# Optimization experiments

Hardware: AMD Instinct MI355X
Metric: run time of the kernel (lower is better)

The kernel has to match this reference:

```python
import jax, jax.numpy as jnp
import numpy as np


def setup_inputs() -> dict:
    key = jax.random.key(0)
    k1, k2, k3, k4 = jax.random.split(key, 4)
    B, L, P = 1024, 128, 32
    ctrl_latent = jax.random.normal(k1, (B, L), dtype=jnp.float32)
    pert_embedding = jax.random.normal(k2, (B, P), dtype=jnp.float32)
    # learned params (torch init is zeros; use small randn so grads/outputs are non-trivial)
    weights = jax.random.normal(k3, (L * P * P, L), dtype=jnp.float32) * 0.02
    bias = jax.random.normal(k4, (L,), dtype=jnp.float32) * 0.02
    return {"ctrl_latent": ctrl_latent, "pert_embedding": pert_embedding,
            "weights": weights, "bias": bias}


def reference(ctrl_latent, pert_embedding, weights, bias):
    # ctrl_latent: (B, L); pert_embedding: (B, P); weights: (L*P*P, L); bias: (L,)
    B = ctrl_latent.shape[0]
    # outer product of pert embedding with itself: (B, P, P) -> (B, P*P)
    inter = jnp.einsum('bi,bj->bij', pert_embedding, pert_embedding).reshape(B, -1)
    # full interaction with control latent: (B, L, P*P) -> (B, L*P*P)
    x = (ctrl_latent[:, :, None] * inter[:, None, :]).reshape(B, -1)
    # dropout is identity at inference
    return x @ weights + bias
```

## Files before the change

kernel.cpp:

```cpp
#include <hip/hip_runtime.h>
#include <hip/hip_bf16.h>
#include <hip/hip_fp16.h>

#define B_   1024
#define L_   128
#define P_   32
#define PP_  1024
#define N_   128
#define KP_  576
#define KT_  73728

typedef float    f32x4 __attribute__((ext_vector_type(4)));
typedef _Float16 f16x8 __attribute__((ext_vector_type(8)));
typedef _Float16 f16x2 __attribute__((ext_vector_type(2)));
typedef __fp16   fp16x2_builtin __attribute__((ext_vector_type(2)));

__device__ __constant__ unsigned char IJTAB[36] = {
  0,1,2,3,4,5,6,7, 9,10,11,12,13,14,15, 18,19,20,21,22,23,
  27,28,29,30,31, 36,37,38,39, 45,46,47, 54,55, 63};

static __device__ __forceinline__ unsigned int pk16(float a, float b) {
  fp16x2_builtin h = __builtin_amdgcn_cvt_pkrtz(a, b);
  return *(unsigned int*)&h;
}

static __device__ __forceinline__ void gload16(void* lds, const void* g) {
  __builtin_amdgcn_global_load_lds(
      (const __attribute__((address_space(1))) unsigned int*)g,
      (__attribute__((address_space(3))) unsigned int*)lds, 16, 0, 0);
}

__global__ __launch_bounds__(256) void prep_kernel(
    const float* __restrict__ W, const float* __restrict__ pert,
    unsigned short* __restrict__ Wt, uint4* __restrict__ interf)
{
  const int bid = blockIdx.x, tid = threadIdx.x;
  __shared__ unsigned int t32[32 * 133];
  if (bid < 1152) {
    const int q = bid & 127, grp = bid >> 7;
    const int l = (q & 63) * 2 + (q >> 6);
    const size_t baseL = (size_t)l * PP_;
    for (int i = 0; i < 4; ++i) {
      int idx = tid + i * 256;
      int sp = idx >> 5, nq = (idx & 31) * 4;
      const int s = grp * 64 + 2 * sp;
      const int blk = s >> 4, a = (s >> 2) & 3, c = (s >> 1) & 1;
      const int ij = IJTAB[blk], I = ij >> 3, J = ij & 7;
      const int rowX = (4 * I + a) * 32 + 4 * J + 2 * c;
      float4 s0 = *(const float4*)(W + (baseL + rowX)     * N_ + nq);
      float4 s1 = *(const float4*)(W + (baseL + rowX + 1) * N_ + nq);
      if (I != J) {
        const int rowY0 = (4 * J + 2 * c) * 32 + 4 * I + a;
        const float4 y0 = *(const float4*)(W + (baseL + rowY0)      * N_ + nq);
        const float4 y1 = *(const float4*)(W + (baseL + rowY0 + 32) * N_ + nq);
        s0.x += y0.x; s0.y += y0.y; s0.z += y0.z; s0.w += y0.w;
        s1.x += y1.x; s1.y += y1.y; s1.z += y1.z; s1.w += y1.w;
      }
      uint4 w;
      w.x = pk16(s0.x, s1.x);
      w.y = pk16(s0.y, s1.y);
      w.z = pk16(s0.z, s1.z);
      w.w = pk16(s0.w, s1.w);
      *(uint4*)&t32[sp * 133 + nq] = w;
    }
    __syncthreads();
    for (int i = 0; i < 4; ++i) {
      int idx = tid + i * 256;
      int n = idx >> 3, cg = idx & 7;
      uint4 w;
      w.x = t32[(cg * 4 + 0) * 133 + n];
      w.y = t32[(cg * 4 + 1) * 133 + n];
      w.z = t32[(cg * 4 + 2) * 133 + n];
      w.w = t32[(cg * 4 + 3) * 133 + n];
      *(uint4*)(Wt + (size_t)n * KT_ + l * KP_ + grp * 64 + cg * 8) = w;
    }
  } else {
    const int mt = bid - 1152;
    __shared__ float pl[512];
    pl[tid]       = pert[(size_t)mt * 512 + tid];
    pl[tid + 256] = pert[(size_t)mt * 512 + tid + 256];
    __syncthreads();
    for (int r = 0; r < 5; ++r) {
      const int idx = tid + r * 256;
      if (idx < 1152) {
        const int k8 = idx >> 4, lm = idx & 15;
        const int blk = k8 >> 1, a0 = 2 * (k8 & 1);
        const int ij = IJTAB[blk], I = ij >> 3, J = ij & 7;
        const float* p = &pl[lm * 32];
        const float pi0 = p[4 * I + a0], pi1 = p[4 * I + a0 + 1];
        const float* pj = p + 4 * J;
        uint4 w;
        w.x = pk16(pi0 * pj[0], pi0 * pj[1]);
        w.y = pk16(pi0 * pj[2], pi0 * pj[3]);
        w.z = pk16(pi1 * pj[0], pi1 * pj[1]);
        w.w = pk16(pi1 * pj[2], pi1 * pj[3]);
        interf[(size_t)mt * 1152 + idx] = w;
      }
    }
  }
}

__global__ __launch_bounds__(256, 2) void gemm_kernel(
    const unsigned short* __restrict__ Wt,
    const uint4* __restrict__ interf,
    const float* __restrict__ ctrl,
    _Float16* __restrict__ partials)
{
  __shared__ unsigned short Bsm[2][128 * 64];

  const int tid    = threadIdx.x;
  const int kchunk = blockIdx.x & 63;
  const int mtile  = blockIdx.x >> 6;
  const int m0     = mtile * 128;
  const int l0     = kchunk * 2;
  const int lane = tid & 63, wid = tid >> 6;
  const int wm = (wid >> 1) * 64, wn = (wid & 1) * 64;
  const int lm = lane & 15, kq = lane >> 4;

  const int srow = lane >> 3, c8 = lane & 7;
  const int sc = (c8 ^ srow) * 8;

  const unsigned short* bg0[4]; const unsigned short* bg1[4];
  unsigned short* bl0[4];       unsigned short* bl1[4];
  for (int j = 0; j < 4; ++j) {
    const int rr = wid * 32 + j * 8;
    bg0[j] = Wt + (size_t)(rr + srow) * KT_ + (size_t)l0 * KP_ + sc;
    bg1[j] = bg0[j] + KP_;
    bl0[j] = &Bsm[0][rr * 64];
    bl1[j] = &Bsm[1][rr * 64];
  }

  const uint4* ap[4];
  for (int tm = 0; tm < 4; ++tm)
    ap[tm] = interf + (size_t)(mtile * 8 + (wid >> 1) * 4 + tm) * 1152 + lane;

  f32x4 acc[2][4][4];
  for (int li = 0; li < 2; ++li)
    for (int tm = 0; tm < 4; ++tm)
      for (int tn = 0; tn < 4; ++tn)
        acc[li][tm][tn] = (f32x4){0.f, 0.f, 0.f, 0.f};

  for (int it = 0; it < 9; ++it) {
    const int q0 = it * 64;
    __syncthreads();
    f16x8 af[2][4];
    for (int ks = 0; ks < 2; ++ks)
      for (int tm = 0; tm < 4; ++tm)
        af[ks][tm] = *(const f16x8*)(ap[tm] + it * 128 + ks * 64);
    for (int j = 0; j < 4; ++j) gload16(bl0[j], bg0[j] + q0);
    for (int j = 0; j < 4; ++j) gload16(bl1[j], bg1[j] + q0);
    __syncthreads();
    for (int ks = 0; ks < 2; ++ks) {
      const int ch = (((ks * 4 + kq) ^ (lm & 7)) * 8);
      for (int li = 0; li < 2; ++li) {
        f16x8 bfr[4];
        for (int t = 0; t < 4; ++t)
          bfr[t] = *(const f16x8*)&Bsm[li][(wn + t * 16 + lm) * 64 + ch];
        for (int tm = 0; tm < 4; ++tm)
          for (int t = 0; t < 4; ++t)
            acc[li][tm][t] = __builtin_amdgcn_mfma_f32_16x16x32_f16(
                af[ks][tm], bfr[t], acc[li][tm][t], 0, 0, 0);
      }
    }
  }

  _Float16* pb = partials + (size_t)blockIdx.x * (128 * 128);
  for (int tm = 0; tm < 4; ++tm)
    for (int reg = 0; reg < 4; ++reg) {
      const int row = wm + tm * 16 + kq * 4 + reg;
      const float c0v = ctrl[(size_t)(m0 + row) * L_ + l0];
      const float c1v = ctrl[(size_t)(m0 + row) * L_ + l0 + 1];
      for (int tn = 0; tn < 4; ++tn)
        pb[row * 128 + wn + tn * 16 + lm] = (_Float16)(
            c0v * acc[0][tm][tn][reg] + c1v * acc[1][tm][tn][reg]);
    }
}

__global__ __launch_bounds__(256) void reduce_kernel(
    const _Float16* __restrict__ partials, const float* __restrict__ bias,
    float* __restrict__ out)
{
  __shared__ float red[4][64][2];
  const int bid = blockIdx.x;
  const int mtile = bid >> 7, row = bid & 127;
  const int tid = threadIdx.x, lane = tid & 63, w = tid >> 6;
  const _Float16* base = partials + ((size_t)(mtile * 64)) * 16384
                         + row * 128 + lane * 2;
  float s0 = 0.f, s1 = 0.f;
  #pragma unroll 8
  for (int i = 0; i < 16; ++i) {
    const int sp = w + i * 4;
    f16x2 v = *(const f16x2*)(base + ((size_t)sp << 14));
    s0 += (float)v[0];
    s1 += (float)v[1];
  }
  red[w][lane][0] = s0;
  red[w][lane][1] = s1;
  __syncthreads();
  if (w == 0) {
    float r0 = red[0][lane][0] + red[1][lane][0] + red[2][lane][0] + red[3][lane][0];
    float r1 = red[0][lane][1] + red[1][lane][1] + red[2][lane][1] + red[3][lane][1];
    r0 += bias[lane * 2];
    r1 += bias[lane * 2 + 1];
    float2 o; o.x = r0; o.y = r1;
    *(float2*)(out + (size_t)bid * N_ + lane * 2) = o;
  }
}

__global__ __launch_bounds__(256) void naive_kernel(
    const float* __restrict__ ctrl, const float* __restrict__ pert,
    const float* __restrict__ W, const float* __restrict__ bias,
    float* __restrict__ out)
{
  __shared__ float red[256];
  __shared__ float pl[P_];
  __shared__ float cl[L_];
  const int b = blockIdx.x, t = threadIdx.x;
  if (t < P_)  pl[t] = pert[(size_t)b * P_ + t];
  if (t < L_)  cl[t] = ctrl[(size_t)b * L_ + t];
  __syncthreads();
  const int m = t & 127, half = t >> 7;
  float acc = 0.f;
  for (int l = 0; l < L_; ++l) {
    float c = cl[l];
    for (int qq = half * 512; qq < half * 512 + 512; ++qq) {
      float x = c * pl[qq >> 5] * pl[qq & 31];
      acc += x * W[((size_t)l * PP_ + qq) * N_ + m];
    }
  }
  red[t] = acc;
  __syncthreads();
  if (t < 128) out[(size_t)b * 128 + t] = red[t] + red[t + 128] + bias[t];
}

extern "C" void kernel_launch(void* const* d_in, const int* in_sizes, int n_in,
                              void* d_out, int out_size, void* d_ws, size_t ws_size,
                              hipStream_t stream) {
  const float* ctrl = (const float*)d_in[0];
  const float* pert = (const float*)d_in[1];
  const float* W    = (const float*)d_in[2];
  const float* bias = (const float*)d_in[3];
  float* out = (float*)d_out;

  const size_t offWt    = 0;
  const size_t offInter = (size_t)18 << 20;
  const size_t offPart  = (size_t)20 << 20;
  const size_t needWs   = offPart + (size_t)512 * 128 * 128 * sizeof(_Float16);

  if (ws_size >= needWs) {
    unsigned short* Wt    = (unsigned short*)((char*)d_ws + offWt);
    uint4*          intf  = (uint4*)((char*)d_ws + offInter);
    _Float16*       parts = (_Float16*)((char*)d_ws + offPart);

    prep_kernel<<<1216, 256, 0, stream>>>(W, pert, Wt, intf);
    gemm_kernel<<<512, 256, 0, stream>>>(Wt, intf, ctrl, parts);
    reduce_kernel<<<1024, 256, 0, stream>>>(parts, bias, out);
  } else {
    naive_kernel<<<1024, 256, 0, stream>>>(ctrl, pert, W, bias, out);
  }
}
```

Baseline: 128.2 us.

## Double-buffer weight tiles in LDS and prefetch A fragments across iterations

Splits the shared-memory weight tile into two stages. The next iteration's weight tile (global to LDS) and A fragments (into a second register set) are now issued while MFMA runs on the current stage. This removes one barrier per iteration and hides global load latency behind compute. In exchange, LDS use per block doubles to 64KB and an extra set of A-fragment registers is live, which adds register pressure under the 2-blocks-per-CU launch bound.

```diff
diff --git a/kernel.cpp b/kernel.cpp
--- a/kernel.cpp
+++ b/kernel.cpp
@@ -106,7 +106,7 @@
     const float* __restrict__ ctrl,
     _Float16* __restrict__ partials)
 {
-  __shared__ unsigned short Bsm[2][128 * 64];
+  __shared__ unsigned short Bsm[2][2][128 * 64];
 
   const int tid    = threadIdx.x;
   const int kchunk = blockIdx.x & 63;
@@ -121,13 +121,15 @@
   const int sc = (c8 ^ srow) * 8;
 
   const unsigned short* bg0[4]; const unsigned short* bg1[4];
-  unsigned short* bl0[4];       unsigned short* bl1[4];
+  unsigned short* bl[2][2][4];
   for (int j = 0; j < 4; ++j) {
     const int rr = wid * 32 + j * 8;
     bg0[j] = Wt + (size_t)(rr + srow) * KT_ + (size_t)l0 * KP_ + sc;
     bg1[j] = bg0[j] + KP_;
-    bl0[j] = &Bsm[0][rr * 64];
-    bl1[j] = &Bsm[1][rr * 64];
+    bl[0][0][j] = &Bsm[0][0][rr * 64];
+    bl[0][1][j] = &Bsm[0][1][rr * 64];
+    bl[1][0][j] = &Bsm[1][0][rr * 64];
+    bl[1][1][j] = &Bsm[1][1][rr * 64];
   }
 
   const uint4* ap[4];
@@ -140,29 +142,53 @@
       for (int tn = 0; tn < 4; ++tn)
         acc[li][tm][tn] = (f32x4){0.f, 0.f, 0.f, 0.f};
 
-  for (int it = 0; it < 9; ++it) {
-    const int q0 = it * 64;
-    __syncthreads();
-    f16x8 af[2][4];
-    for (int ks = 0; ks < 2; ++ks)
-      for (int tm = 0; tm < 4; ++tm)
-        af[ks][tm] = *(const f16x8*)(ap[tm] + it * 128 + ks * 64);
-    for (int j = 0; j < 4; ++j) gload16(bl0[j], bg0[j] + q0);
-    for (int j = 0; j < 4; ++j) gload16(bl1[j], bg1[j] + q0);
-    __syncthreads();
-    for (int ks = 0; ks < 2; ++ks) {
-      const int ch = (((ks * 4 + kq) ^ (lm & 7)) * 8);
-      for (int li = 0; li < 2; ++li) {
-        f16x8 bfr[4];
-        for (int t = 0; t < 4; ++t)
-          bfr[t] = *(const f16x8*)&Bsm[li][(wn + t * 16 + lm) * 64 + ch];
-        for (int tm = 0; tm < 4; ++tm)
-          for (int t = 0; t < 4; ++t)
-            acc[li][tm][t] = __builtin_amdgcn_mfma_f32_16x16x32_f16(
-                af[ks][tm], bfr[t], acc[li][tm][t], 0, 0, 0);
-      }
-    }
-  }
+  f16x8 afA[2][4], afB[2][4];
+
+#define STAGE_A(dst, itq) do {                                              \
+    for (int ks = 0; ks < 2; ++ks)                                          \
+      for (int tm = 0; tm < 4; ++tm)                                        \
+        dst[ks][tm] = *(const f16x8*)(ap[tm] + (itq) * 128 + ks * 64);      \
+  } while (0)
+
+#define STAGE_B(st, itq) do {                                               \
+    const int _q0 = (itq) * 64;                                             \
+    for (int j = 0; j < 4; ++j) gload16(bl[st][0][j], bg0[j] + _q0);        \
+    for (int j = 0; j < 4; ++j) gload16(bl[st][1][j], bg1[j] + _q0);        \
+  } while (0)
+
+#define COMPUTE(st, afv) do {                                               \
+    for (int ks = 0; ks < 2; ++ks) {                                        \
+      const int ch = (((ks * 4 + kq) ^ (lm & 7)) * 8);  \
+      for (int li = 0; li < 2; ++li) {                                      \
+        f16x8 bfr[4];                                                       \
+        for (int t = 0; t < 4; ++t)                                         \
+          bfr[t] = *(const f16x8*)&Bsm[st][li][(wn + t * 16 + lm) * 64 + ch];\
+        for (int tm = 0; tm < 4; ++tm)                                      \
+          for (int t = 0; t < 4; ++t)                                       \
+            acc[li][tm][t] = __builtin_amdgcn_mfma_f32_16x16x32_f16(        \
+                afv[ks][tm], bfr[t], acc[li][tm][t], 0, 0, 0);              \
+      }                                                                     \
+    }                                                                       \
+  } while (0)
+
+  STAGE_A(afA, 0);
+  STAGE_B(0, 0);
+  __syncthreads();
+  for (int ith = 0; ith < 4; ++ith) {
+    STAGE_A(afB, 2 * ith + 1);
+    STAGE_B(1, 2 * ith + 1);
+    COMPUTE(0, afA);
+    __syncthreads();
+    STAGE_A(afA, 2 * ith + 2);
+    STAGE_B(0, 2 * ith + 2);
+    COMPUTE(1, afB);
+    __syncthreads();
+  }
+  COMPUTE(0, afA);
+
+#undef STAGE_A
+#undef STAGE_B
+#undef COMPUTE
 
   _Float16* pb = partials + (size_t)blockIdx.x * (128 * 128);
   for (int tm = 0; tm < 4; ++tm)
```

Result: no change. 130.3 us (+1.6%).
